# Optimization experiments

Measured on AMD Instinct MI355X. Metric: run time of the kernel, lower is better.

The kernel has to match this reference:

```python
import jax, jax.numpy as jnp
import numpy as np

B, S, IN, DM, H, L, FF, DO, E, K = 512, 64, 128, 256, 8, 2, 1024, 64, 8, 2
HD = DM // H
GI = S * IN


def _ln(x, g, b):
    m = x.mean(-1, keepdims=True)
    v = ((x - m) ** 2).mean(-1, keepdims=True)
    return (x - m) / jnp.sqrt(v + 1e-5) * g + b


def setup_inputs() -> dict:
    key = jax.random.key(0)
    keys = iter(jax.random.split(key, 24))
    rn = lambda shape, scale: jax.random.normal(next(keys), shape, dtype=jnp.float32) * scale
    inp = {
        'x': rn((B, S, IN), 1.0),
        'Win': rn((E, IN, DM), IN ** -0.5), 'bin_': jnp.zeros((E, DM), jnp.float32),
        'Wq': rn((E, L, DM, DM), DM ** -0.5), 'bq': jnp.zeros((E, L, DM), jnp.float32),
        'Wk': rn((E, L, DM, DM), DM ** -0.5), 'bk': jnp.zeros((E, L, DM), jnp.float32),
        'Wv': rn((E, L, DM, DM), DM ** -0.5), 'bv': jnp.zeros((E, L, DM), jnp.float32),
        'Wo': rn((E, L, DM, DM), DM ** -0.5), 'bo': jnp.zeros((E, L, DM), jnp.float32),
        'ln1_g': jnp.ones((E, L, DM), jnp.float32), 'ln1_b': jnp.zeros((E, L, DM), jnp.float32),
        'ln2_g': jnp.ones((E, L, DM), jnp.float32), 'ln2_b': jnp.zeros((E, L, DM), jnp.float32),
        'W1': rn((E, L, DM, FF), DM ** -0.5), 'b1': jnp.zeros((E, L, FF), jnp.float32),
        'W2': rn((E, L, FF, DM), FF ** -0.5), 'b2': jnp.zeros((E, L, DM), jnp.float32),
        'Wout': rn((E, DM, DO), DM ** -0.5), 'bout': jnp.zeros((E, DO), jnp.float32),
        'Wg': rn((GI, E), GI ** -0.5), 'bg': jnp.zeros((E,), jnp.float32),
        'Wr': rn((GI, DO), GI ** -0.5), 'br': jnp.zeros((DO,), jnp.float32),
        'on_g': jnp.ones((DO,), jnp.float32), 'on_b': jnp.zeros((DO,), jnp.float32),
    }
    return inp


def _moe_forward(x, Win, bin_, Wq, bq, Wk, bk, Wv, bv, Wo, bo,
                 ln1_g, ln1_b, ln2_g, ln2_b, W1, b1, W2, b2, Wout, bout,
                 Wg, bg, Wr, br, on_g, on_b):
    gi = x.reshape(B, -1)                       # [B, S*IN] gate input
    logits = gi @ Wg + bg                       # [B, E]
    topk_w, topk_idx = jax.lax.top_k(logits, K)  # [B, K]
    topk_w = jax.nn.softmax(topk_w, axis=-1)
    # combined per-expert weight (dispatch/weighted-combine of _dispatch_to_experts)
    cw = (topk_w[..., None] * jax.nn.one_hot(topk_idx, E, dtype=topk_w.dtype)).sum(1)  # [B, E]

    def one_expert(p):
        h = x @ p['Win'] + p['bin_']            # [B, S, DM]
        for l in range(L):
            q = (h @ p['Wq'][l] + p['bq'][l]).reshape(B, S, H, HD)
            k_ = (h @ p['Wk'][l] + p['bk'][l]).reshape(B, S, H, HD)
            v_ = (h @ p['Wv'][l] + p['bv'][l]).reshape(B, S, H, HD)
            scores = jnp.einsum('bqhd,bkhd->bhqk', q, k_) * (HD ** -0.5)
            attn = jax.nn.softmax(scores, axis=-1)
            av = jnp.einsum('bhqk,bkhd->bqhd', attn, v_).reshape(B, S, DM)
            h = _ln(h + av @ p['Wo'][l] + p['bo'][l], p['ln1_g'][l], p['ln1_b'][l])
            ff = jax.nn.relu(h @ p['W1'][l] + p['b1'][l]) @ p['W2'][l] + p['b2'][l]
            h = _ln(h + ff, p['ln2_g'][l], p['ln2_b'][l])
        return h.mean(axis=1) @ p['Wout'] + p['bout']  # [B, DO]

    params = {'Win': Win, 'bin_': bin_, 'Wq': Wq, 'bq': bq, 'Wk': Wk, 'bk': bk,
              'Wv': Wv, 'bv': bv, 'Wo': Wo, 'bo': bo, 'ln1_g': ln1_g, 'ln1_b': ln1_b,
              'ln2_g': ln2_g, 'ln2_b': ln2_b, 'W1': W1, 'b1': b1, 'W2': W2, 'b2': b2,
              'Wout': Wout, 'bout': bout}
    expert_out = jax.vmap(one_expert)(params)   # [E, B, DO]
    out = jnp.einsum('ebd,be->bd', expert_out, cw)
    out = out + 0.1 * (gi @ Wr + br)            # residual_proj path
    return _ln(out, on_g, on_b)                 # output_norm (eval: no dropout)


def reference(x, Win, bin_, Wq, bq, Wk, bk, Wv, bv, Wo, bo,
              ln1_g, ln1_b, ln2_g, ln2_b, W1, b1, W2, b2, Wout, bout,
              Wg, bg, Wr, br, on_g, on_b):
    return _moe_forward(x, Win, bin_, Wq, bq, Wk, bk, Wv, bv, Wo, bo,
                        ln1_g, ln1_b, ln2_g, ln2_b, W1, b1, W2, b2, Wout, bout,
                        Wg, bg, Wr, br, on_g, on_b)
```

## Files before the change

### kernel.cpp

```cpp
#include <hip/hip_runtime.h>
#include <hip/hip_bf16.h>


typedef __attribute__((ext_vector_type(8))) short bf16x8;
typedef __attribute__((ext_vector_type(4))) float f32x4;

#define DEVINL __device__ __forceinline__
#define MFMA16(a, b, c) __builtin_amdgcn_mfma_f32_16x16x32_bf16((a), (b), (c), 0, 0, 0)

DEVINL float b2f(unsigned short u) {
    unsigned int i = ((unsigned int)u) << 16;
    float f; __builtin_memcpy(&f, &i, 4); return f;
}
DEVINL unsigned short f2b(float f) {
    unsigned int i; __builtin_memcpy(&i, &f, 4);
    unsigned int r = (i + 0x7FFFu + ((i >> 16) & 1u)) >> 16;
    return (unsigned short)r;
}

DEVINL void convT_tile(const float* __restrict__ src, short* __restrict__ dst,
                       int R, int C, int t, int tid)
{
    const int tiles_r = R >> 6, tiles_c = C >> 6;
    const int bM = t / (tiles_r * tiles_c);
    int rem = t - bM * (tiles_r * tiles_c);
    const int tr = rem / tiles_c, tc = rem - tr * tiles_c;
    const int r0 = tr << 6, c0 = tc << 6;
    const float* S = src + (size_t)bM * R * C;
    short* D = dst + (size_t)bM * R * C;
    __shared__ short tile[64][72];
    const int lc = tid & 63;
    const int l0 = tid >> 6;
    #pragma unroll
    for (int i = 0; i < 16; ++i) {
        int lr = l0 * 16 + i;
        tile[lr][lc] = (short)f2b(S[(size_t)(r0 + lr) * C + c0 + lc]);
    }
    __syncthreads();
    #pragma unroll
    for (int i = 0; i < 16; ++i) {
        int lcw = l0 * 16 + i;
        D[(size_t)(c0 + lcw) * R + r0 + lc] = tile[lc][lcw];
    }
}

__global__ __launch_bounds__(256) void convT_fused_kernel(
    const float* __restrict__ Win, short* __restrict__ WinT,
    const float* __restrict__ Wq,  short* __restrict__ WqT,
    const float* __restrict__ Wk,  short* __restrict__ WkT,
    const float* __restrict__ Wv,  short* __restrict__ WvT,
    const float* __restrict__ Wo,  short* __restrict__ WoT,
    const float* __restrict__ W1,  short* __restrict__ W1T,
    const float* __restrict__ W2,  short* __restrict__ W2T,
    int* __restrict__ cnt)
{
    const int tid = threadIdx.x;
    int t = blockIdx.x;
    if (t == 0 && tid < 8) cnt[tid] = 0;
    if (t < 64)        { convT_tile(Win, WinT, 128, 256, t, tid); return; }
    t -= 64;
    if (t < 256)       { convT_tile(Wq, WqT, 256, 256, t, tid); return; }
    t -= 256;
    if (t < 256)       { convT_tile(Wk, WkT, 256, 256, t, tid); return; }
    t -= 256;
    if (t < 256)       { convT_tile(Wv, WvT, 256, 256, t, tid); return; }
    t -= 256;
    if (t < 256)       { convT_tile(Wo, WoT, 256, 256, t, tid); return; }
    t -= 256;
    if (t < 1024)      { convT_tile(W1, W1T, 256, 1024, t, tid); return; }
    t -= 1024;
    convT_tile(W2, W2T, 1024, 256, t, tid);
}

__global__ __launch_bounds__(256) void gate_kernel(
    const float* __restrict__ x, const float* __restrict__ Wg, const float* __restrict__ bg,
    int* __restrict__ cnt, int* __restrict__ rlist, float* __restrict__ wlist)
{
    const int b = blockIdx.x;
    const int tid = threadIdx.x;
    const int e8 = tid & 7;
    const int seg = tid >> 3;
    const float* gi = x + (size_t)b * 8192;
    double p = 0.0;
    for (int ii = 0; ii < 256; ++ii) {
        int i = seg * 256 + ii;
        p += (double)gi[i] * (double)Wg[i * 8 + e8];
    }
    p += __shfl_xor(p, 8, 64);
    p += __shfl_xor(p, 16, 64);
    p += __shfl_xor(p, 32, 64);
    __shared__ double wred[4 * 8];
    const int lane = tid & 63, w = tid >> 6;
    if (lane < 8) wred[w * 8 + lane] = p;
    __syncthreads();
    if (tid == 0) {
        double lg[8];
        for (int e = 0; e < 8; ++e)
            lg[e] = wred[e] + wred[8 + e] + wred[16 + e] + wred[24 + e] + (double)bg[e];
        int i1 = 0;
        for (int e = 1; e < 8; ++e) if (lg[e] > lg[i1]) i1 = e;
        int i2 = (i1 == 0) ? 1 : 0;
        for (int e = 0; e < 8; ++e) if (e != i1 && lg[e] > lg[i2]) i2 = e;
        double ex = exp(lg[i2] - lg[i1]);
        float w1 = (float)(1.0 / (1.0 + ex));
        float w2 = (float)(ex / (1.0 + ex));
        int p1 = atomicAdd(&cnt[i1], 1);
        rlist[i1 * 512 + p1] = b; wlist[i1 * 512 + p1] = w1;
        int p2 = atomicAdd(&cnt[i2], 1);
        rlist[i2 * 512 + p2] = b; wlist[i2 * 512 + p2] = w2;
    }
}

__global__ __launch_bounds__(256) void resproj_kernel(
    const float* __restrict__ x, const float* __restrict__ Wr, const float* __restrict__ br,
    float* __restrict__ acc_out)
{
    const int b0 = blockIdx.x * 2;
    const int tid = threadIdx.x;
    const int d = tid & 63;
    const int part = tid >> 6;
    float acc0 = 0.f, acc1 = 0.f;
    for (int ii = 0; ii < 2048; ++ii) {
        int i = part * 2048 + ii;
        float wv = Wr[i * 64 + d];
        acc0 += x[(size_t)b0 * 8192 + i] * wv;
        acc1 += x[(size_t)(b0 + 1) * 8192 + i] * wv;
    }
    __shared__ float rr[4][2][64];
    rr[part][0][d] = acc0;
    rr[part][1][d] = acc1;
    __syncthreads();
    if (tid < 128) {
        int k = tid >> 6, dd = tid & 63;
        float v = rr[0][k][dd] + rr[1][k][dd] + rr[2][k][dd] + rr[3][k][dd];
        acc_out[(b0 + k) * 64 + dd] = 0.1f * (v + br[dd]);
    }
}

__global__ __launch_bounds__(256, 2) void expert_kernel(
    const float* __restrict__ x,
    const short* __restrict__ WinT, const float* __restrict__ bin_,
    const short* __restrict__ WqT,  const float* __restrict__ bq,
    const short* __restrict__ WkT,  const float* __restrict__ bk,
    const short* __restrict__ WvT,  const float* __restrict__ bv,
    const short* __restrict__ WoT,  const float* __restrict__ bo,
    const float* __restrict__ ln1g, const float* __restrict__ ln1b,
    const float* __restrict__ ln2g, const float* __restrict__ ln2b,
    const short* __restrict__ W1T,  const float* __restrict__ b1,
    const short* __restrict__ W2T,  const float* __restrict__ b2,
    const float* __restrict__ Wout, const float* __restrict__ bout,
    const int* __restrict__ cnt, const int* __restrict__ rlist,
    const float* __restrict__ wlist, float* __restrict__ acc_out)
{
    const int e = blockIdx.x & 7;
    const int s = blockIdx.x >> 3;
    if (s >= cnt[e]) return;
    const int b   = rlist[e * 512 + s];
    const float wgt = wlist[e * 512 + s];
    const int tid = threadIdx.x;
    const int lane = tid & 63;
    const int wg  = __builtin_amdgcn_readfirstlane(tid >> 6);
    const int ln = lane & 15, quad = lane >> 4;
    const int nb = wg * 64;

    __shared__ __align__(16) unsigned short hS[64 * 264];
    __shared__ __align__(16) unsigned short attnS[4 * 5184];
    __shared__ float redS[512];
    __shared__ float pooledS[256];
    unsigned short* VTw   = attnS + wg * 5184;
    unsigned short* Qw    = VTw + 2304;
    unsigned short* Kpart = VTw + 4608;
    unsigned short* PSw   = Qw;
    unsigned short* xS    = attnS;

    {
        const float* xb = x + (size_t)b * 8192;
        #pragma unroll
        for (int i = 0; i < 32; ++i) {
            int id = tid + 256 * i;
            xS[(id >> 7) * 136 + (id & 127)] = f2b(xb[id]);
        }
    }
    __syncthreads();

    f32x4 hr[16];

    {
        const short* BW = WinT + (size_t)e * 32768;
        const float* bp = bin_ + e * 256;
        #pragma unroll
        for (int ct = 0; ct < 4; ++ct) {
            bf16x8 Bf[4];
            #pragma unroll
            for (int kt = 0; kt < 4; ++kt)
                Bf[kt] = *(const bf16x8*)(BW + (size_t)(nb + ct * 16 + ln) * 128 + kt * 32 + quad * 8);
            const float bz = bp[nb + ct * 16 + ln];
            #pragma unroll
            for (int rt = 0; rt < 4; ++rt) {
                bf16x8 Af[4];
                #pragma unroll
                for (int kt = 0; kt < 4; ++kt)
                    Af[kt] = *(const bf16x8*)&xS[(rt * 16 + ln) * 136 + kt * 32 + quad * 8];
                f32x4 c = {bz, bz, bz, bz};
                #pragma unroll
                for (int kt = 0; kt < 4; ++kt) c = MFMA16(Af[kt], Bf[kt], c);
                hr[rt * 4 + ct] = c;
                #pragma unroll
                for (int i = 0; i < 4; ++i)
                    hS[(rt * 16 + quad * 4 + i) * 264 + nb + ct * 16 + ln] = f2b(c[i]);
            }
        }
    }
    __syncthreads();

    auto LN = [&](f32x4* a, const float* g, const float* bb) {
        #pragma unroll
        for (int rt = 0; rt < 4; ++rt)
            #pragma unroll
            for (int i = 0; i < 4; ++i) {
                float s1 = 0.f, s2 = 0.f;
                #pragma unroll
                for (int ct = 0; ct < 4; ++ct) { float v = a[rt * 4 + ct][i]; s1 += v; s2 += v * v; }
                s1 += __shfl_xor(s1, 1); s1 += __shfl_xor(s1, 2);
                s1 += __shfl_xor(s1, 4); s1 += __shfl_xor(s1, 8);
                s2 += __shfl_xor(s2, 1); s2 += __shfl_xor(s2, 2);
                s2 += __shfl_xor(s2, 4); s2 += __shfl_xor(s2, 8);
                if (ln == 0) {
                    int row = rt * 16 + quad * 4 + i;
                    redS[row * 8 + wg * 2] = s1;
                    redS[row * 8 + wg * 2 + 1] = s2;
                }
            }
        __syncthreads();
        float gv[4], bv2[4];
        #pragma unroll
        for (int ct = 0; ct < 4; ++ct) { gv[ct] = g[nb + ct * 16 + ln]; bv2[ct] = bb[nb + ct * 16 + ln]; }
        #pragma unroll
        for (int rt = 0; rt < 4; ++rt)
            #pragma unroll
            for (int i = 0; i < 4; ++i) {
                int row = rt * 16 + quad * 4 + i;
                float S1 = redS[row * 8 + 0] + redS[row * 8 + 2] + redS[row * 8 + 4] + redS[row * 8 + 6];
                float S2 = redS[row * 8 + 1] + redS[row * 8 + 3] + redS[row * 8 + 5] + redS[row * 8 + 7];
                float m_ = S1 * (1.f / 256.f);
                float rstd = rsqrtf(S2 * (1.f / 256.f) - m_ * m_ + 1e-5f);
                #pragma unroll
                for (int ct = 0; ct < 4; ++ct) {
                    float v = (a[rt * 4 + ct][i] - m_) * rstd * gv[ct] + bv2[ct];
                    hr[rt * 4 + ct][i] = v;
                    hS[row * 264 + nb + ct * 16 + ln] = f2b(v);
                }
            }
        __syncthreads();
    };

    for (int l = 0; l < 2; ++l) {
        const int el = e * 2 + l;
        const short* WqE = WqT + (size_t)el * 65536;
        const short* WkE = WkT + (size_t)el * 65536;
        const short* WvE = WvT + (size_t)el * 65536;
        const short* WoE = WoT + (size_t)el * 65536;
        const short* W1E = W1T + (size_t)el * 262144;
        const short* W2E = W2T + (size_t)el * 262144;
        const float* bq_p = bq + el * 256;
        const float* bk_p = bk + el * 256;
        const float* bv_p = bv + el * 256;
        const float* bo_p = bo + el * 256;

        f32x4 avr[16];

        #pragma unroll
        for (int hp = 0; hp < 2; ++hp) {
            const int hb = nb + hp * 32;

            #pragma unroll
            for (int ct2 = 0; ct2 < 2; ++ct2) {
                bf16x8 Bq[8];
                #pragma unroll
                for (int kt = 0; kt < 8; ++kt)
                    Bq[kt] = *(const bf16x8*)(WvE + (size_t)(hb + ct2 * 16 + ln) * 256 + kt * 32 + quad * 8);
                const float bz2 = bv_p[hb + ct2 * 16 + ln];
                #pragma unroll
                for (int rt = 0; rt < 4; ++rt) {
                    bf16x8 Af[8];
                    #pragma unroll
                    for (int kt = 0; kt < 8; ++kt)
                        Af[kt] = *(const bf16x8*)&hS[(rt * 16 + ln) * 264 + kt * 32 + quad * 8];
                    f32x4 c = {bz2, bz2, bz2, bz2};
                    #pragma unroll
                    for (int kt = 0; kt < 8; ++kt) c = MFMA16(Af[kt], Bq[kt], c);
                    #pragma unroll
                    for (int i = 0; i < 4; ++i)
                        VTw[(ct2 * 16 + ln) * 72 + rt * 16 + quad * 4 + i] = f2b(c[i]);
                }
            }

            #pragma unroll
            for (int ct2 = 0; ct2 < 2; ++ct2) {
                bf16x8 Bq[8];
                #pragma unroll
                for (int kt = 0; kt < 8; ++kt)
                    Bq[kt] = *(const bf16x8*)(WqE + (size_t)(hb + ct2 * 16 + ln) * 256 + kt * 32 + quad * 8);
                const float bz2 = bq_p[hb + ct2 * 16 + ln];
                #pragma unroll
                for (int rt = 0; rt < 4; ++rt) {
                    bf16x8 Af[8];
                    #pragma unroll
                    for (int kt = 0; kt < 8; ++kt)
                        Af[kt] = *(const bf16x8*)&hS[(rt * 16 + ln) * 264 + kt * 32 + quad * 8];
                    f32x4 c = {bz2, bz2, bz2, bz2};
                    #pragma unroll
                    for (int kt = 0; kt < 8; ++kt) c = MFMA16(Af[kt], Bq[kt], c);
                    #pragma unroll
                    for (int i = 0; i < 4; ++i)
                        Qw[(rt * 16 + quad * 4 + i) * 36 + ct2 * 16 + ln] = f2b(c[i]);
                }
            }

            f32x4 sc[16];
            {
                float bkz[2];
                #pragma unroll
                for (int ct2 = 0; ct2 < 2; ++ct2) bkz[ct2] = bk_p[hb + ct2 * 16 + ln];
                #pragma unroll
                for (int ck = 0; ck < 4; ++ck) {
                    bf16x8 Af[8];
                    #pragma unroll
                    for (int kt = 0; kt < 8; ++kt)
                        Af[kt] = *(const bf16x8*)&hS[(ck * 16 + ln) * 264 + kt * 32 + quad * 8];
                    #pragma unroll
                    for (int ct2 = 0; ct2 < 2; ++ct2) {
                        bf16x8 WkB[8];
                        #pragma unroll
                        for (int kt = 0; kt < 8; ++kt)
                            WkB[kt] = *(const bf16x8*)(WkE + (size_t)(hb + ct2 * 16 + ln) * 256 + kt * 32 + quad * 8);
                        f32x4 c = {bkz[ct2], bkz[ct2], bkz[ct2], bkz[ct2]};
                        #pragma unroll
                        for (int kt = 0; kt < 8; ++kt) c = MFMA16(Af[kt], WkB[kt], c);
                        #pragma unroll
                        for (int i = 0; i < 4; ++i)
                            Kpart[(quad * 4 + i) * 36 + ct2 * 16 + ln] = f2b(c[i]);
                    }
                    bf16x8 Bk = *(const bf16x8*)&Kpart[ln * 36 + quad * 8];
                    #pragma unroll
                    for (int rt = 0; rt < 4; ++rt) {
                        bf16x8 Aq = *(const bf16x8*)&Qw[(rt * 16 + ln) * 36 + quad * 8];
                        f32x4 z = {0.f, 0.f, 0.f, 0.f};
                        sc[rt * 4 + ck] = MFMA16(Aq, Bk, z);
                    }
                }
            }

            const float sscale = 0.17677669529663687f;
            #pragma unroll
            for (int t = 0; t < 16; ++t)
                #pragma unroll
                for (int i = 0; i < 4; ++i) sc[t][i] *= sscale;
            #pragma unroll
            for (int rt = 0; rt < 4; ++rt)
                #pragma unroll
                for (int i = 0; i < 4; ++i) {
                    float m_ = fmaxf(fmaxf(sc[rt * 4 + 0][i], sc[rt * 4 + 1][i]),
                                     fmaxf(sc[rt * 4 + 2][i], sc[rt * 4 + 3][i]));
                    m_ = fmaxf(m_, __shfl_xor(m_, 1));
                    m_ = fmaxf(m_, __shfl_xor(m_, 2));
                    m_ = fmaxf(m_, __shfl_xor(m_, 4));
                    m_ = fmaxf(m_, __shfl_xor(m_, 8));
                    float s_ = 0.f;
                    #pragma unroll
                    for (int ck = 0; ck < 4; ++ck) {
                        sc[rt * 4 + ck][i] = __expf(sc[rt * 4 + ck][i] - m_);
                        s_ += sc[rt * 4 + ck][i];
                    }
                    s_ += __shfl_xor(s_, 1); s_ += __shfl_xor(s_, 2);
                    s_ += __shfl_xor(s_, 4); s_ += __shfl_xor(s_, 8);
                    float inv = 1.f / s_;
                    #pragma unroll
                    for (int ck = 0; ck < 4; ++ck) sc[rt * 4 + ck][i] *= inv;
                }

            #pragma unroll
            for (int rt = 0; rt < 4; ++rt)
                #pragma unroll
                for (int i = 0; i < 4; ++i)
                    #pragma unroll
                    for (int ck = 0; ck < 2; ++ck)
                        PSw[(rt * 16 + quad * 4 + i) * 36 + ck * 16 + ln] = f2b(sc[rt * 4 + ck][i]);
            {
                bf16x8 Bv0[2];
                #pragma unroll
                for (int ct2 = 0; ct2 < 2; ++ct2)
                    Bv0[ct2] = *(const bf16x8*)&VTw[(ct2 * 16 + ln) * 72 + quad * 8];
                #pragma unroll
                for (int rt = 0; rt < 4; ++rt) {
                    bf16x8 Ap = *(const bf16x8*)&PSw[(rt * 16 + ln) * 36 + quad * 8];
                    #pragma unroll
                    for (int ct2 = 0; ct2 < 2; ++ct2) {
                        f32x4 z = {0.f, 0.f, 0.f, 0.f};
                        avr[hp * 8 + rt * 2 + ct2] = MFMA16(Ap, Bv0[ct2], z);
                    }
                }
            }
            #pragma unroll
            for (int rt = 0; rt < 4; ++rt)
                #pragma unroll
                for (int i = 0; i < 4; ++i)
                    #pragma unroll
                    for (int ck = 2; ck < 4; ++ck)
                        PSw[(rt * 16 + quad * 4 + i) * 36 + (ck - 2) * 16 + ln] = f2b(sc[rt * 4 + ck][i]);
            {
                bf16x8 Bv1[2];
                #pragma unroll
                for (int ct2 = 0; ct2 < 2; ++ct2)
                    Bv1[ct2] = *(const bf16x8*)&VTw[(ct2 * 16 + ln) * 72 + 32 + quad * 8];
                #pragma unroll
                for (int rt = 0; rt < 4; ++rt) {
                    bf16x8 Ap = *(const bf16x8*)&PSw[(rt * 16 + ln) * 36 + quad * 8];
                    #pragma unroll
                    for (int ct2 = 0; ct2 < 2; ++ct2)
                        avr[hp * 8 + rt * 2 + ct2] = MFMA16(Ap, Bv1[ct2], avr[hp * 8 + rt * 2 + ct2]);
                }
            }
        }

        __syncthreads();
        #pragma unroll
        for (int hp = 0; hp < 2; ++hp)
            #pragma unroll
            for (int rt = 0; rt < 4; ++rt)
                #pragma unroll
                for (int ct2 = 0; ct2 < 2; ++ct2)
                    #pragma unroll
                    for (int i = 0; i < 4; ++i)
                        hS[(rt * 16 + quad * 4 + i) * 264 + nb + hp * 32 + ct2 * 16 + ln]
                            = f2b(avr[hp * 8 + rt * 2 + ct2][i]);
        __syncthreads();

        f32x4 oacc[16];
        #pragma unroll
        for (int rt = 0; rt < 4; ++rt)
            #pragma unroll
            for (int ct = 0; ct < 4; ++ct) {
                float bz = bo_p[nb + ct * 16 + ln];
                f32x4 t = hr[rt * 4 + ct];
                t[0] += bz; t[1] += bz; t[2] += bz; t[3] += bz;
                oacc[rt * 4 + ct] = t;
            }
        #pragma unroll
        for (int ct = 0; ct < 4; ++ct) {
            bf16x8 Bo[8];
            #pragma unroll
            for (int kt = 0; kt < 8; ++kt)
                Bo[kt] = *(const bf16x8*)(WoE + (size_t)(nb + ct * 16 + ln) * 256 + kt * 32 + quad * 8);
            #pragma unroll
            for (int rt = 0; rt < 4; ++rt) {
                bf16x8 Ao[8];
                #pragma unroll
                for (int kt = 0; kt < 8; ++kt)
                    Ao[kt] = *(const bf16x8*)&hS[(rt * 16 + ln) * 264 + kt * 32 + quad * 8];
                #pragma unroll
                for (int kt = 0; kt < 8; ++kt)
                    oacc[rt * 4 + ct] = MFMA16(Ao[kt], Bo[kt], oacc[rt * 4 + ct]);
            }
        }

        LN(oacc, ln1g + el * 256, ln1b + el * 256);

        f32x4 facc[16];
        {
            const float* b2_p = b2 + el * 256;
            #pragma unroll
            for (int rt = 0; rt < 4; ++rt)
                #pragma unroll
                for (int ct = 0; ct < 4; ++ct) {
                    float bz = b2_p[nb + ct * 16 + ln];
                    f32x4 t = hr[rt * 4 + ct];
                    t[0] += bz; t[1] += bz; t[2] += bz; t[3] += bz;
                    facc[rt * 4 + ct] = t;
                }
        }
        const float* b1_p = b1 + el * 1024;
        for (int ch = 0; ch < 8; ++ch) {
            const int fb = ch * 128 + wg * 32;
            unsigned short* tC = attnS + (ch & 1) * 8704;
            #pragma unroll
            for (int ct2 = 0; ct2 < 2; ++ct2) {
                bf16x8 B1c[8];
                #pragma unroll
                for (int kt = 0; kt < 8; ++kt)
                    B1c[kt] = *(const bf16x8*)(W1E + (size_t)(fb + ct2 * 16 + ln) * 256 + kt * 32 + quad * 8);
                const float bz2 = b1_p[fb + ct2 * 16 + ln];
                #pragma unroll
                for (int rt = 0; rt < 4; ++rt) {
                    bf16x8 Af[8];
                    #pragma unroll
                    for (int kt = 0; kt < 8; ++kt)
                        Af[kt] = *(const bf16x8*)&hS[(rt * 16 + ln) * 264 + kt * 32 + quad * 8];
                    f32x4 c = {bz2, bz2, bz2, bz2};
                    #pragma unroll
                    for (int kt = 0; kt < 8; ++kt) c = MFMA16(Af[kt], B1c[kt], c);
                    #pragma unroll
                    for (int i = 0; i < 4; ++i)
                        tC[(rt * 16 + quad * 4 + i) * 136 + wg * 32 + ct2 * 16 + ln]
                            = f2b(fmaxf(c[i], 0.f));
                }
            }
            __syncthreads();
            #pragma unroll
            for (int ct = 0; ct < 4; ++ct) {
                bf16x8 B2c[4];
                #pragma unroll
                for (int kt2 = 0; kt2 < 4; ++kt2)
                    B2c[kt2] = *(const bf16x8*)(W2E + (size_t)(nb + ct * 16 + ln) * 1024 + ch * 128 + kt2 * 32 + quad * 8);
                #pragma unroll
                for (int rt = 0; rt < 4; ++rt) {
                    bf16x8 At[4];
                    #pragma unroll
                    for (int kt2 = 0; kt2 < 4; ++kt2)
                        At[kt2] = *(const bf16x8*)&tC[(rt * 16 + ln) * 136 + kt2 * 32 + quad * 8];
                    #pragma unroll
                    for (int kt2 = 0; kt2 < 4; ++kt2)
                        facc[rt * 4 + ct] = MFMA16(At[kt2], B2c[kt2], facc[rt * 4 + ct]);
                }
            }
        }

        LN(facc, ln2g + el * 256, ln2b + el * 256);
    }

    {
        #pragma unroll
        for (int ct = 0; ct < 4; ++ct) {
            float s_ = 0.f;
            #pragma unroll
            for (int rt = 0; rt < 4; ++rt)
                #pragma unroll
                for (int i = 0; i < 4; ++i) s_ += hr[rt * 4 + ct][i];
            s_ += __shfl_xor(s_, 16);
            s_ += __shfl_xor(s_, 32);
            if (quad == 0) pooledS[nb + ct * 16 + ln] = s_ * (1.f / 64.f);
        }
        __syncthreads();
        if (tid < 64) {
            const float* Wout_p = Wout + (size_t)e * (256 * 64);
            float o = bout[e * 64 + tid];
            for (int c = 0; c < 256; ++c) o += pooledS[c] * Wout_p[c * 64 + tid];
            atomicAdd(&acc_out[b * 64 + tid], wgt * o);
        }
    }
}

__global__ __launch_bounds__(64) void final_ln_kernel(
    const float* __restrict__ acc_out, const float* __restrict__ on_g,
    const float* __restrict__ on_b, float* __restrict__ out)
{
    const int b = blockIdx.x;
    const int d = threadIdx.x;
    float v = acc_out[b * 64 + d];
    float s1 = v, s2 = v * v;
    #pragma unroll
    for (int st = 1; st < 64; st <<= 1) {
        s1 += __shfl_xor(s1, st, 64);
        s2 += __shfl_xor(s2, st, 64);
    }
    float m   = s1 * (1.f / 64.f);
    float var = s2 * (1.f / 64.f) - m * m;
    float rstd = rsqrtf(var + 1e-5f);
    out[b * 64 + d] = (v - m) * rstd * on_g[d] + on_b[d];
}

extern "C" void kernel_launch(void* const* d_in, const int* in_sizes, int n_in,
                              void* d_out, int out_size, void* d_ws, size_t ws_size,
                              hipStream_t stream)
{
    (void)in_sizes; (void)n_in; (void)out_size; (void)ws_size;
    const float* x    = (const float*)d_in[0];
    const float* Win  = (const float*)d_in[1];
    const float* bin_ = (const float*)d_in[2];
    const float* Wq   = (const float*)d_in[3];
    const float* bq   = (const float*)d_in[4];
    const float* Wk   = (const float*)d_in[5];
    const float* bk   = (const float*)d_in[6];
    const float* Wv   = (const float*)d_in[7];
    const float* bv   = (const float*)d_in[8];
    const float* Wo   = (const float*)d_in[9];
    const float* bo   = (const float*)d_in[10];
    const float* ln1g = (const float*)d_in[11];
    const float* ln1b = (const float*)d_in[12];
    const float* ln2g = (const float*)d_in[13];
    const float* ln2b = (const float*)d_in[14];
    const float* W1   = (const float*)d_in[15];
    const float* b1   = (const float*)d_in[16];
    const float* W2   = (const float*)d_in[17];
    const float* b2   = (const float*)d_in[18];
    const float* Wout = (const float*)d_in[19];
    const float* bout = (const float*)d_in[20];
    const float* Wg   = (const float*)d_in[21];
    const float* bg   = (const float*)d_in[22];
    const float* Wr   = (const float*)d_in[23];
    const float* br   = (const float*)d_in[24];
    const float* on_g = (const float*)d_in[25];
    const float* on_b = (const float*)d_in[26];
    float* out = (float*)d_out;

    char* ws = (char*)d_ws;
    float* acc_out = (float*)ws;
    int*   cnt     = (int*)(ws + 131072);
    int*   rlist   = (int*)(ws + 131200);
    float* wlist   = (float*)(ws + 147584);
    short* WinT    = (short*)(ws + 164096);
    short* WqT     = (short*)(ws + 688384);
    short* WkT     = (short*)(ws + 2785536);
    short* WvT     = (short*)(ws + 4882688);
    short* WoT     = (short*)(ws + 6979840);
    short* W1T     = (short*)(ws + 9076992);
    short* W2T     = (short*)(ws + 17465600);

    convT_fused_kernel<<<3136, 256, 0, stream>>>(
        Win, WinT, Wq, WqT, Wk, WkT, Wv, WvT, Wo, WoT, W1, W1T, W2, W2T, cnt);

    gate_kernel<<<512, 256, 0, stream>>>(x, Wg, bg, cnt, rlist, wlist);
    resproj_kernel<<<256, 256, 0, stream>>>(x, Wr, br, acc_out);
    expert_kernel<<<4096, 256, 0, stream>>>(x,
        WinT, bin_, WqT, bq, WkT, bk, WvT, bv, WoT, bo,
        ln1g, ln1b, ln2g, ln2b, W1T, b1, W2T, b2, Wout, bout,
        cnt, rlist, wlist, acc_out);
    final_ln_kernel<<<512, 64, 0, stream>>>(acc_out, on_g, on_b, out);
}
```

Before: 1.006 ms.

## Fuse gate and residual projection into prep and expert kernels

Gate computation and acc_out zeroing move into the weight-transpose prep kernel as extra blocks. The residual projection runs as 256 extra blocks of the expert kernel, accumulating with atomicAdd into the zeroed acc_out. A tiny kernel zeroes the counters first. This removes separate launches and lets independent work overlap, at the cost of atomics on acc_out and one extra tiny launch.

```diff
diff --git a/kernel.cpp b/kernel.cpp
--- a/kernel.cpp
+++ b/kernel.cpp
@@ -18,8 +18,12 @@
     return (unsigned short)r;
 }
 
+__global__ void zero_cnt_kernel(int* __restrict__ cnt) {
+    if (threadIdx.x < 8) cnt[threadIdx.x] = 0;
+}
+
 DEVINL void convT_tile(const float* __restrict__ src, short* __restrict__ dst,
-                       int R, int C, int t, int tid)
+                       int R, int C, int t, int tid, short (*tile)[72])
 {
     const int tiles_r = R >> 6, tiles_c = C >> 6;
     const int bM = t / (tiles_r * tiles_c);
@@ -28,7 +32,6 @@
     const int r0 = tr << 6, c0 = tc << 6;
     const float* S = src + (size_t)bM * R * C;
     short* D = dst + (size_t)bM * R * C;
-    __shared__ short tile[64][72];
     const int lc = tid & 63;
     const int l0 = tid >> 6;
     #pragma unroll
@@ -44,7 +47,7 @@
     }
 }
 
-__global__ __launch_bounds__(256) void convT_fused_kernel(
+__global__ __launch_bounds__(256) void prep_fused_kernel(
     const float* __restrict__ Win, short* __restrict__ WinT,
     const float* __restrict__ Wq,  short* __restrict__ WqT,
     const float* __restrict__ Wk,  short* __restrict__ WkT,
@@ -52,89 +55,66 @@
     const float* __restrict__ Wo,  short* __restrict__ WoT,
     const float* __restrict__ W1,  short* __restrict__ W1T,
     const float* __restrict__ W2,  short* __restrict__ W2T,
-    int* __restrict__ cnt)
+    const float* __restrict__ x,   const float* __restrict__ Wg,
+    const float* __restrict__ bg,  int* __restrict__ cnt,
+    int* __restrict__ rlist, float* __restrict__ wlist,
+    float* __restrict__ acc_out)
 {
+    __shared__ short tile[64][72];
+    __shared__ double wred[4 * 8];
     const int tid = threadIdx.x;
     int t = blockIdx.x;
-    if (t == 0 && tid < 8) cnt[tid] = 0;
-    if (t < 64)        { convT_tile(Win, WinT, 128, 256, t, tid); return; }
+    if (t < 64)   { convT_tile(Win, WinT, 128, 256, t, tid, tile); return; }
     t -= 64;
-    if (t < 256)       { convT_tile(Wq, WqT, 256, 256, t, tid); return; }
+    if (t < 256)  { convT_tile(Wq, WqT, 256, 256, t, tid, tile); return; }
     t -= 256;
-    if (t < 256)       { convT_tile(Wk, WkT, 256, 256, t, tid); return; }
+    if (t < 256)  { convT_tile(Wk, WkT, 256, 256, t, tid, tile); return; }
     t -= 256;
-    if (t < 256)       { convT_tile(Wv, WvT, 256, 256, t, tid); return; }
+    if (t < 256)  { convT_tile(Wv, WvT, 256, 256, t, tid, tile); return; }
     t -= 256;
-    if (t < 256)       { convT_tile(Wo, WoT, 256, 256, t, tid); return; }
+    if (t < 256)  { convT_tile(Wo, WoT, 256, 256, t, tid, tile); return; }
     t -= 256;
-    if (t < 1024)      { convT_tile(W1, W1T, 256, 1024, t, tid); return; }
+    if (t < 1024) { convT_tile(W1, W1T, 256, 1024, t, tid, tile); return; }
     t -= 1024;
-    convT_tile(W2, W2T, 1024, 256, t, tid);
-}
-
-__global__ __launch_bounds__(256) void gate_kernel(
-    const float* __restrict__ x, const float* __restrict__ Wg, const float* __restrict__ bg,
-    int* __restrict__ cnt, int* __restrict__ rlist, float* __restrict__ wlist)
-{
-    const int b = blockIdx.x;
-    const int tid = threadIdx.x;
-    const int e8 = tid & 7;
-    const int seg = tid >> 3;
-    const float* gi = x + (size_t)b * 8192;
-    double p = 0.0;
-    for (int ii = 0; ii < 256; ++ii) {
-        int i = seg * 256 + ii;
-        p += (double)gi[i] * (double)Wg[i * 8 + e8];
-    }
-    p += __shfl_xor(p, 8, 64);
-    p += __shfl_xor(p, 16, 64);
-    p += __shfl_xor(p, 32, 64);
-    __shared__ double wred[4 * 8];
-    const int lane = tid & 63, w = tid >> 6;
-    if (lane < 8) wred[w * 8 + lane] = p;
-    __syncthreads();
-    if (tid == 0) {
-        double lg[8];
-        for (int e = 0; e < 8; ++e)
-            lg[e] = wred[e] + wred[8 + e] + wred[16 + e] + wred[24 + e] + (double)bg[e];
-        int i1 = 0;
-        for (int e = 1; e < 8; ++e) if (lg[e] > lg[i1]) i1 = e;
-        int i2 = (i1 == 0) ? 1 : 0;
-        for (int e = 0; e < 8; ++e) if (e != i1 && lg[e] > lg[i2]) i2 = e;
-        double ex = exp(lg[i2] - lg[i1]);
-        float w1 = (float)(1.0 / (1.0 + ex));
-        float w2 = (float)(ex / (1.0 + ex));
-        int p1 = atomicAdd(&cnt[i1], 1);
-        rlist[i1 * 512 + p1] = b; wlist[i1 * 512 + p1] = w1;
-        int p2 = atomicAdd(&cnt[i2], 1);
-        rlist[i2 * 512 + p2] = b; wlist[i2 * 512 + p2] = w2;
-    }
-}
-
-__global__ __launch_bounds__(256) void resproj_kernel(
-    const float* __restrict__ x, const float* __restrict__ Wr, const float* __restrict__ br,
-    float* __restrict__ acc_out)
-{
-    const int b0 = blockIdx.x * 2;
-    const int tid = threadIdx.x;
-    const int d = tid & 63;
-    const int part = tid >> 6;
-    float acc0 = 0.f, acc1 = 0.f;
-    for (int ii = 0; ii < 2048; ++ii) {
-        int i = part * 2048 + ii;
-        float wv = Wr[i * 64 + d];
-        acc0 += x[(size_t)b0 * 8192 + i] * wv;
-        acc1 += x[(size_t)(b0 + 1) * 8192 + i] * wv;
-    }
-    __shared__ float rr[4][2][64];
-    rr[part][0][d] = acc0;
-    rr[part][1][d] = acc1;
-    __syncthreads();
-    if (tid < 128) {
-        int k = tid >> 6, dd = tid & 63;
-        float v = rr[0][k][dd] + rr[1][k][dd] + rr[2][k][dd] + rr[3][k][dd];
-        acc_out[(b0 + k) * 64 + dd] = 0.1f * (v + br[dd]);
-    }
+    if (t < 1024) { convT_tile(W2, W2T, 1024, 256, t, tid, tile); return; }
+    t -= 1024;
+    if (t < 512) {
+        const int b = t;
+        const int e8 = tid & 7;
+        const int seg = tid >> 3;
+        const float* gi = x + (size_t)b * 8192;
+        double p = 0.0;
+        for (int ii = 0; ii < 256; ++ii) {
+            int i = seg * 256 + ii;
+            p += (double)gi[i] * (double)Wg[i * 8 + e8];
+        }
+        p += __shfl_xor(p, 8, 64);
+        p += __shfl_xor(p, 16, 64);
+        p += __shfl_xor(p, 32, 64);
+        const int lane = tid & 63, w = tid >> 6;
+        if (lane < 8) wred[w * 8 + lane] = p;
+        __syncthreads();
+        if (tid == 0) {
+            double lg[8];
+            for (int e = 0; e < 8; ++e)
+                lg[e] = wred[e] + wred[8 + e] + wred[16 + e] + wred[24 + e] + (double)bg[e];
+            int i1 = 0;
+            for (int e = 1; e < 8; ++e) if (lg[e] > lg[i1]) i1 = e;
+            int i2 = (i1 == 0) ? 1 : 0;
+            for (int e = 0; e < 8; ++e) if (e != i1 && lg[e] > lg[i2]) i2 = e;
+            double ex = exp(lg[i2] - lg[i1]);
+            float w1 = (float)(1.0 / (1.0 + ex));
+            float w2 = (float)(ex / (1.0 + ex));
+            int p1 = atomicAdd(&cnt[i1], 1);
+            rlist[i1 * 512 + p1] = b; wlist[i1 * 512 + p1] = w1;
+            int p2 = atomicAdd(&cnt[i2], 1);
+            rlist[i2 * 512 + p2] = b; wlist[i2 * 512 + p2] = w2;
+        }
+        return;
+    }
+    t -= 512;
+    f32x4 z = {0.f, 0.f, 0.f, 0.f};
+    ((f32x4*)acc_out)[t * 256 + tid] = z;
 }
 
 __global__ __launch_bounds__(256, 2) void expert_kernel(
@@ -149,24 +129,50 @@
     const short* __restrict__ W1T,  const float* __restrict__ b1,
     const short* __restrict__ W2T,  const float* __restrict__ b2,
     const float* __restrict__ Wout, const float* __restrict__ bout,
+    const float* __restrict__ Wr,   const float* __restrict__ br,
     const int* __restrict__ cnt, const int* __restrict__ rlist,
     const float* __restrict__ wlist, float* __restrict__ acc_out)
 {
+    __shared__ __align__(16) unsigned short hS[64 * 264];
+    __shared__ __align__(16) unsigned short attnS[4 * 5184];
+    __shared__ float redS[512];
+    __shared__ float pooledS[256];
+
+    const int tid = threadIdx.x;
+
+    if (blockIdx.x >= 4096) {
+        const int b0 = (blockIdx.x - 4096) * 2;
+        const int d = tid & 63;
+        const int part = tid >> 6;
+        float acc0 = 0.f, acc1 = 0.f;
+        for (int ii = 0; ii < 2048; ++ii) {
+            int i = part * 2048 + ii;
+            float wv = Wr[i * 64 + d];
+            acc0 += x[(size_t)b0 * 8192 + i] * wv;
+            acc1 += x[(size_t)(b0 + 1) * 8192 + i] * wv;
+        }
+        float (*rr)[2][64] = (float(*)[2][64])redS;
+        rr[part][0][d] = acc0;
+        rr[part][1][d] = acc1;
+        __syncthreads();
+        if (tid < 128) {
+            int k = tid >> 6, dd = tid & 63;
+            float v = rr[0][k][dd] + rr[1][k][dd] + rr[2][k][dd] + rr[3][k][dd];
+            atomicAdd(&acc_out[(b0 + k) * 64 + dd], 0.1f * (v + br[dd]));
+        }
+        return;
+    }
+
     const int e = blockIdx.x & 7;
     const int s = blockIdx.x >> 3;
     if (s >= cnt[e]) return;
     const int b   = rlist[e * 512 + s];
     const float wgt = wlist[e * 512 + s];
-    const int tid = threadIdx.x;
     const int lane = tid & 63;
     const int wg  = __builtin_amdgcn_readfirstlane(tid >> 6);
     const int ln = lane & 15, quad = lane >> 4;
     const int nb = wg * 64;
 
-    __shared__ __align__(16) unsigned short hS[64 * 264];
-    __shared__ __align__(16) unsigned short attnS[4 * 5184];
-    __shared__ float redS[512];
-    __shared__ float pooledS[256];
     unsigned short* VTw   = attnS + wg * 5184;
     unsigned short* Qw    = VTw + 2304;
     unsigned short* Kpart = VTw + 4608;
@@ -616,14 +622,13 @@
     short* W1T     = (short*)(ws + 9076992);
     short* W2T     = (short*)(ws + 17465600);
 
-    convT_fused_kernel<<<3136, 256, 0, stream>>>(
-        Win, WinT, Wq, WqT, Wk, WkT, Wv, WvT, Wo, WoT, W1, W1T, W2, W2T, cnt);
-
-    gate_kernel<<<512, 256, 0, stream>>>(x, Wg, bg, cnt, rlist, wlist);
-    resproj_kernel<<<256, 256, 0, stream>>>(x, Wr, br, acc_out);
-    expert_kernel<<<4096, 256, 0, stream>>>(x,
+    zero_cnt_kernel<<<1, 64, 0, stream>>>(cnt);
+    prep_fused_kernel<<<3680, 256, 0, stream>>>(
+        Win, WinT, Wq, WqT, Wk, WkT, Wv, WvT, Wo, WoT, W1, W1T, W2, W2T,
+        x, Wg, bg, cnt, rlist, wlist, acc_out);
+    expert_kernel<<<4352, 256, 0, stream>>>(x,
         WinT, bin_, WqT, bq, WkT, bk, WvT, bv, WoT, bo,
-        ln1g, ln1b, ln2g, ln2b, W1T, b1, W2T, b2, Wout, bout,
+        ln1g, ln1b, ln2g, ln2b, W1T, b1, W2T, b2, Wout, bout, Wr, br,
         cnt, rlist, wlist, acc_out);
     final_ln_kernel<<<512, 64, 0, stream>>>(acc_out, on_g, on_b, out);
 }
```

Result: faster. 877.5 us (-12.8%).
